# Performance work log

Measured on AMD Instinct MI355X. Metric: run time of the kernel, lower is better.

## Reference

```python
import jax, jax.numpy as jnp
import numpy as np

T1 = 8      # list[index-1]
T2 = 8      # list[index]
L = 8
GAMA = 1.0
EPS = -8e-05

@jax.custom_vjp
def zif(u):
    return (u >= EPS).astype(u.dtype)

def _zif_fwd(u):
    return zif(u), u

def _zif_bwd(u, g):
    tmp = (1.0 / GAMA) * (1.0 / GAMA) * jnp.clip(GAMA - jnp.abs(u), a_min=0.0)
    return (g * tmp,)

zif.defvjp(_zif_fwd, _zif_bwd)


def setup_inputs() -> dict:
    key = jax.random.key(0)
    k1, k2 = jax.random.split(key)
    x = jax.random.uniform(k1, (T1 * 32, 128, 32, 32), dtype=jnp.float32)
    thresh = jnp.ones((1,), dtype=jnp.float32)  # nn.Parameter([1.0])
    return {"x": x, "thresh": thresh}


def _if_forward(x, thresh):
    # thre = thresh.data / L  (detached in the original)
    thre = jax.lax.stop_gradient(thresh) / L          # [1]
    # expand: [T1*B, C, H, W] -> [T1, B, C, H, W]
    B = x.shape[0] // T1
    x_seq = x.reshape((T1, B) + x.shape[1:])
    frame_shape = x_seq.shape[1:]

    mem0 = jnp.broadcast_to(0.5 * thre, frame_shape).astype(x.dtype)
    sc0 = jnp.zeros(frame_shape, dtype=x.dtype)

    # Phase 1: integrate-and-fire over the T1 input frames
    def step1(carry, xt):
        mem, sc = carry
        mem = mem + xt
        spike = zif(mem - thre) * thre
        mem = mem - spike
        return (mem, sc + spike), None
    (mem, sc), _ = jax.lax.scan(step1, (mem0, sc0), x_seq)

    # Phase 2: T3-1 relaxation steps with reverse spikes (hard, no surrogate)
    T3 = max(T1, T2)
    def step2(carry, _):
        mem, sc = carry
        spike = zif(mem - thre) * thre
        rev = (-mem > 0).astype(mem.dtype) * thre
        mem = mem - spike + rev
        return (mem, sc + spike - rev), None
    (mem, sc), _ = jax.lax.scan(step2, (mem, sc), None, length=T3 - 1)

    # Phase 3: re-emit spike_count as T2 output spikes
    def step3(mem, _):
        spike = zif(mem - thre) * thre
        return mem - spike, spike
    _, spike_pot = jax.lax.scan(step3, sc, None, length=T2)  # [T2, B, C, H, W]

    # merge: flatten(0, 1)
    return spike_pot.reshape((T2 * B,) + frame_shape[1:])


def reference(x, thresh):
    return _if_forward(x, thresh)
```

## Files before the change

### kernel.cpp

```cpp
#include <hip/hip_runtime.h>


#define T1 8
#define T2 8
#define L_DIV 8.0f
#define EPS_C (-8e-05f)

typedef float fvec4 __attribute__((ext_vector_type(4)));

__global__ __launch_bounds__(256) void if_fwd_kernel(
    const fvec4* __restrict__ x,
    const float* __restrict__ thresh,
    fvec4* __restrict__ out,
    int n4)
{
    const int i = blockIdx.x * blockDim.x + threadIdx.x;

    const float thre = thresh[0] / L_DIV;

    const fvec4* a0 = &x[(size_t)0 * n4 + i];
    const fvec4* a1 = &x[(size_t)1 * n4 + i];
    const fvec4* a2 = &x[(size_t)2 * n4 + i];
    const fvec4* a3 = &x[(size_t)3 * n4 + i];
    const fvec4* a4 = &x[(size_t)4 * n4 + i];
    const fvec4* a5 = &x[(size_t)5 * n4 + i];
    const fvec4* a6 = &x[(size_t)6 * n4 + i];
    const fvec4* a7 = &x[(size_t)7 * n4 + i];

    fvec4 xv[T1];
    asm volatile(
        "global_load_dwordx4 %0, %8, off\n\t"
        "global_load_dwordx4 %1, %9, off\n\t"
        "global_load_dwordx4 %2, %10, off\n\t"
        "global_load_dwordx4 %3, %11, off\n\t"
        "global_load_dwordx4 %4, %12, off\n\t"
        "global_load_dwordx4 %5, %13, off\n\t"
        "global_load_dwordx4 %6, %14, off\n\t"
        "global_load_dwordx4 %7, %15, off\n\t"
        "s_waitcnt vmcnt(0)"
        : "=&v"(xv[0]), "=&v"(xv[1]), "=&v"(xv[2]), "=&v"(xv[3]),
          "=&v"(xv[4]), "=&v"(xv[5]), "=&v"(xv[6]), "=&v"(xv[7])
        : "v"(a0), "v"(a1), "v"(a2), "v"(a3),
          "v"(a4), "v"(a5), "v"(a6), "v"(a7)
        : "memory");

    float m[4], sc[4];
    #pragma unroll
    for (int k = 0; k < 4; ++k) { m[k] = 0.5f * thre; sc[k] = 0.0f; }

    #pragma unroll
    for (int t = 0; t < T1; ++t) {
        #pragma unroll
        for (int k = 0; k < 4; ++k) {
            m[k] += xv[t][k];
            const float spike = (m[k] - thre >= EPS_C) ? thre : 0.0f;
            m[k] -= spike;
            sc[k] += spike;
        }
    }

    #pragma unroll
    for (int t = 0; t < T1 - 1; ++t) {
        #pragma unroll
        for (int k = 0; k < 4; ++k) {
            const float spike = (m[k] - thre >= EPS_C) ? thre : 0.0f;
            const float rev   = (-m[k] > 0.0f) ? thre : 0.0f;
            m[k] = m[k] - spike + rev;
            sc[k] += spike - rev;
        }
    }

    #pragma unroll
    for (int t = 0; t < T2; ++t) {
        fvec4 o;
        #pragma unroll
        for (int k = 0; k < 4; ++k) {
            const float spike = (sc[k] - thre >= EPS_C) ? thre : 0.0f;
            o[k] = spike;
            sc[k] -= spike;
        }
        __builtin_nontemporal_store(o, &out[(size_t)t * n4 + i]);
    }
}

extern "C" void kernel_launch(void* const* d_in, const int* in_sizes, int n_in,
                              void* d_out, int out_size, void* d_ws, size_t ws_size,
                              hipStream_t stream) {
    const fvec4* x      = (const fvec4*)d_in[0];
    const float* thresh = (const float*)d_in[1];
    fvec4*       out    = (fvec4*)d_out;

    const int N  = in_sizes[0] / T1;
    const int n4 = N / 4;

    const int block = 256;
    const int grid  = n4 / block;
    if_fwd_kernel<<<grid, block, 0, stream>>>(x, thresh, out, n4);
}
```

Baseline: 245.0 us.

## Split into phase-1/2 and phase-3 kernels via workspace, with fused fallback

When workspace is large enough, the single kernel becomes two. The first reads the inputs and writes the per-element spike counts to workspace, and the second reads those counts and emits the eight output frames. This separates the read-heavy and write-heavy phases so each kernel streams in one direction. The cost is an extra round trip through memory for the counts plus a second launch. A fallback fused kernel handles two vec4 elements per thread with plain loads for more memory-level parallelism.

```diff
diff --git a/kernel.cpp b/kernel.cpp
--- a/kernel.cpp
+++ b/kernel.cpp
@@ -8,14 +8,13 @@
 
 typedef float fvec4 __attribute__((ext_vector_type(4)));
 
-__global__ __launch_bounds__(256) void if_fwd_kernel(
+__global__ __launch_bounds__(256) void if_phase12_kernel(
     const fvec4* __restrict__ x,
     const float* __restrict__ thresh,
-    fvec4* __restrict__ out,
+    fvec4* __restrict__ sc_out,
     int n4)
 {
     const int i = blockIdx.x * blockDim.x + threadIdx.x;
-
     const float thre = thresh[0] / L_DIV;
 
     const fvec4* a0 = &x[(size_t)0 * n4 + i];
@@ -70,6 +69,24 @@
         }
     }
 
+    fvec4 o;
+    #pragma unroll
+    for (int k = 0; k < 4; ++k) o[k] = sc[k];
+    sc_out[i] = o;
+}
+
+__global__ __launch_bounds__(256) void if_phase3_kernel(
+    const fvec4* __restrict__ sc_in,
+    const float* __restrict__ thresh,
+    fvec4* __restrict__ out,
+    int n4)
+{
+    const int i = blockIdx.x * blockDim.x + threadIdx.x;
+    const float thre = thresh[0] / L_DIV;
+
+    const fvec4 scv = sc_in[i];
+    float sc[4] = {scv[0], scv[1], scv[2], scv[3]};
+
     #pragma unroll
     for (int t = 0; t < T2; ++t) {
         fvec4 o;
@@ -83,6 +100,68 @@
     }
 }
 
+#define G 2
+__global__ __launch_bounds__(256) void if_fused_kernel(
+    const fvec4* __restrict__ x,
+    const float* __restrict__ thresh,
+    fvec4* __restrict__ out,
+    int n4)
+{
+    const int base = blockIdx.x * (blockDim.x * G) + threadIdx.x;
+    const float thre = thresh[0] / L_DIV;
+
+    fvec4 xv[G][T1];
+    #pragma unroll
+    for (int t = 0; t < T1; ++t)
+        #pragma unroll
+        for (int g = 0; g < G; ++g)
+            xv[g][t] = x[(size_t)t * n4 + base + g * 256];
+
+    float m[G][4], sc[G][4];
+    #pragma unroll
+    for (int g = 0; g < G; ++g)
+        #pragma unroll
+        for (int k = 0; k < 4; ++k) { m[g][k] = 0.5f * thre; sc[g][k] = 0.0f; }
+
+    #pragma unroll
+    for (int t = 0; t < T1; ++t)
+        #pragma unroll
+        for (int g = 0; g < G; ++g)
+            #pragma unroll
+            for (int k = 0; k < 4; ++k) {
+                m[g][k] += xv[g][t][k];
+                const float spike = (m[g][k] - thre >= EPS_C) ? thre : 0.0f;
+                m[g][k] -= spike;
+                sc[g][k] += spike;
+            }
+
+    #pragma unroll
+    for (int t = 0; t < T1 - 1; ++t)
+        #pragma unroll
+        for (int g = 0; g < G; ++g)
+            #pragma unroll
+            for (int k = 0; k < 4; ++k) {
+                const float spike = (m[g][k] - thre >= EPS_C) ? thre : 0.0f;
+                const float rev   = (-m[g][k] > 0.0f) ? thre : 0.0f;
+                m[g][k] = m[g][k] - spike + rev;
+                sc[g][k] += spike - rev;
+            }
+
+    #pragma unroll
+    for (int t = 0; t < T2; ++t)
+        #pragma unroll
+        for (int g = 0; g < G; ++g) {
+            fvec4 o;
+            #pragma unroll
+            for (int k = 0; k < 4; ++k) {
+                const float spike = (sc[g][k] - thre >= EPS_C) ? thre : 0.0f;
+                o[k] = spike;
+                sc[g][k] -= spike;
+            }
+            __builtin_nontemporal_store(o, &out[(size_t)t * n4 + base + g * 256]);
+        }
+}
+
 extern "C" void kernel_launch(void* const* d_in, const int* in_sizes, int n_in,
                               void* d_out, int out_size, void* d_ws, size_t ws_size,
                               hipStream_t stream) {
@@ -92,8 +171,17 @@
 
     const int N  = in_sizes[0] / T1;
     const int n4 = N / 4;
+    const int block = 256;
 
-    const int block = 256;
-    const int grid  = n4 / block;
-    if_fwd_kernel<<<grid, block, 0, stream>>>(x, thresh, out, n4);
+    const size_t sc_bytes = (size_t)N * sizeof(float);
+
+    if (ws_size >= sc_bytes) {
+        fvec4* sc = (fvec4*)d_ws;
+        const int grid = n4 / block;
+        if_phase12_kernel<<<grid, block, 0, stream>>>(x, thresh, sc, n4);
+        if_phase3_kernel<<<grid, block, 0, stream>>>(sc, thresh, out, n4);
+    } else {
+        const int grid = n4 / (block * G);
+        if_fused_kernel<<<grid, block, 0, stream>>>(x, thresh, out, n4);
+    }
 }
```

Result: slower. 250.0 us (+2.0%).
